# Kernel optimization log

Hardware: AMD Instinct MI355X
Metric: run time of the kernel (lower is better)

The kernel has to match this reference:

```python
import jax, jax.numpy as jnp
import numpy as np


def setup_inputs() -> dict:
    key = jax.random.key(0)
    ks = jax.random.split(key, 8)
    T, B, I, H = 512, 64, 512, 1024
    def xavier(k, shape):
        fan_in, fan_out = shape[1], shape[0]
        bound = float(np.sqrt(6.0 / (fan_in + fan_out)))
        return jax.random.uniform(k, shape, jnp.float32, -bound, bound)
    return {
        "x_seq": jax.random.normal(ks[0], (T, B, I), jnp.float32),
        "h0": jax.random.normal(ks[1], (B, H), jnp.float32),
        "U_c": xavier(ks[2], (H, I)),
        "W_c": xavier(ks[3], (H, H)),
        "b_c": jnp.zeros((H,), jnp.float32),
        "U_a": xavier(ks[4], (H, I)),
        "W_a": xavier(ks[5], (H, H)),
        "b_a": jnp.zeros((H,), jnp.float32),
        "U_h": xavier(ks[6], (H, I)),
        "b_h": jnp.zeros((H,), jnp.float32),
    }


def reference(x_seq, h0, U_c, W_c, b_c, U_a, W_a, b_a, U_h, b_h):
    # Precompute input projections for all timesteps in one big GEMM each:
    # [T, B, I] x [I, H] -> [T, B, H]
    xc = jnp.einsum('tbi,hi->tbh', x_seq, U_c) + b_c
    xa = jnp.einsum('tbi,hi->tbh', x_seq, U_a) + b_a
    xh = jnp.einsum('tbi,hi->tbh', x_seq, U_h) + b_h

    def step(h, xs):
        xc_t, xa_t, xh_t = xs
        c = jax.nn.sigmoid(xc_t + h @ W_c.T)           # [B, H]
        a = 1.0 + jnp.tanh(xa_t + h @ W_a.T)            # [B, H]
        h_new = c * h + (1.0 - c) * jnp.tanh(xh_t + a * h)
        return h_new, h_new

    h_final, y_seq = jax.lax.scan(step, h0, (xc, xa, xh))
    return y_seq, h_final
```

## Files before the change

### kernel.cpp

```cpp
#include <hip/hip_runtime.h>
#include <stdint.h>

typedef unsigned short u16;
typedef unsigned int u32;
typedef unsigned long long u64;
typedef short short8 __attribute__((ext_vector_type(8)));
typedef float f32x4 __attribute__((ext_vector_type(4)));
typedef float f32x2 __attribute__((ext_vector_type(2)));

#define T_STEPS 512
#define BATCH 64
#define IDIM 512
#define HDIM 1024
#define TBm (T_STEPS*BATCH)
#define N3 (3*HDIM)
#define NBLK 128

__device__ __forceinline__ float bf2f(u16 s) {
  union { u32 u; float f; } v; v.u = ((u32)s) << 16; return v.f;
}
__device__ __forceinline__ u16 f2b(float f) {
  union { float f; u32 u; } v; v.f = f;
  u32 u = v.u;
  u += 0x7fffu + ((u >> 16) & 1u);
  return (u16)(u >> 16);
}
__device__ __forceinline__ float ftanh(float x) {
  x = fminf(20.f, fmaxf(-20.f, x));
  float e = __expf(2.f * x);
  return (e - 1.f) / (e + 1.f);
}
__device__ __forceinline__ float fsigm(float x) {
  x = fminf(30.f, fmaxf(-30.f, x));
  return 1.f / (1.f + __expf(-x));
}

__global__ void split_f32(const float* __restrict__ src, u16* __restrict__ hi,
                          u16* __restrict__ lo, int n4) {
  int i = blockIdx.x * blockDim.x + threadIdx.x;
  if (i >= n4) return;
  float4 a = ((const float4*)src)[i];
  u16 h0 = f2b(a.x), h1 = f2b(a.y), h2 = f2b(a.z), h3 = f2b(a.w);
  u16 l0 = f2b(a.x - bf2f(h0)), l1 = f2b(a.y - bf2f(h1));
  u16 l2 = f2b(a.z - bf2f(h2)), l3 = f2b(a.w - bf2f(h3));
  uint2 hv; hv.x = (u32)h0 | ((u32)h1 << 16); hv.y = (u32)h2 | ((u32)h3 << 16);
  uint2 lv; lv.x = (u32)l0 | ((u32)l1 << 16); lv.y = (u32)l2 | ((u32)l3 << 16);
  ((uint2*)hi)[i] = hv;
  ((uint2*)lo)[i] = lv;
}

__global__ void ws_small_kernel(float* out, int n, float val) {
  int i = blockIdx.x * blockDim.x + threadIdx.x;
  for (; i < n; i += gridDim.x * blockDim.x) out[i] = val;
}

template<typename PT>
__global__ __launch_bounds__(256) void proj_gemm(const u16* __restrict__ Xh, const u16* __restrict__ Xl,
                                                 const u16* __restrict__ Uh, const u16* __restrict__ Ul,
                                                 const float* __restrict__ bias,
                                                 PT* __restrict__ Pb) {
  __shared__ u16 Ash[4096], Asl[4096], Bsh[4096], Bsl[4096];
  const int tid = threadIdx.x;
  const int bm = blockIdx.x, bn = blockIdx.y;
  const int w = tid >> 6, l = tid & 63;
  const int wm = w >> 1, wn = w & 1;
  const int lr = l & 15, kg = l >> 4;

  const int r0t = tid >> 2;
  const int kc = tid & 3;
  const size_t ga0 = (size_t)(bm * 128 + r0t) * IDIM + kc * 8;
  const size_t ga1 = ga0 + (size_t)64 * IDIM;
  const size_t gb0 = (size_t)(bn * 128 + r0t) * IDIM + kc * 8;
  const size_t gb1 = gb0 + (size_t)64 * IDIM;
  const int la0 = (kc * 128 + r0t) * 8;
  const int la1 = la0 + 64 * 8;

  uint4 rah0 = *(const uint4*)(Xh + ga0);
  uint4 rah1 = *(const uint4*)(Xh + ga1);
  uint4 ral0 = *(const uint4*)(Xl + ga0);
  uint4 ral1 = *(const uint4*)(Xl + ga1);
  uint4 rbh0 = *(const uint4*)(Uh + gb0);
  uint4 rbh1 = *(const uint4*)(Uh + gb1);
  uint4 rbl0 = *(const uint4*)(Ul + gb0);
  uint4 rbl1 = *(const uint4*)(Ul + gb1);

  const f32x4 vz = {0.f, 0.f, 0.f, 0.f};
  f32x4 acc[4][4];
#pragma unroll
  for (int i = 0; i < 4; i++)
#pragma unroll
    for (int j = 0; j < 4; j++) acc[i][j] = vz;

  for (int kt = 0; kt < 16; kt++) {
    *(uint4*)&Ash[la0] = rah0; *(uint4*)&Ash[la1] = rah1;
    *(uint4*)&Asl[la0] = ral0; *(uint4*)&Asl[la1] = ral1;
    *(uint4*)&Bsh[la0] = rbh0; *(uint4*)&Bsh[la1] = rbh1;
    *(uint4*)&Bsl[la0] = rbl0; *(uint4*)&Bsl[la1] = rbl1;
    __syncthreads();
    if (kt < 15) {
      size_t ko = (size_t)(kt + 1) * 32;
      rah0 = *(const uint4*)(Xh + ga0 + ko); rah1 = *(const uint4*)(Xh + ga1 + ko);
      ral0 = *(const uint4*)(Xl + ga0 + ko); ral1 = *(const uint4*)(Xl + ga1 + ko);
      rbh0 = *(const uint4*)(Uh + gb0 + ko); rbh1 = *(const uint4*)(Uh + gb1 + ko);
      rbl0 = *(const uint4*)(Ul + gb0 + ko); rbl1 = *(const uint4*)(Ul + gb1 + ko);
    }
    short8 afh[4], afl[4], bfh[4], bfl[4];
#pragma unroll
    for (int mt = 0; mt < 4; mt++) {
      int idx = (kg * 128 + wm * 64 + mt * 16 + lr) * 8;
      afh[mt] = *(const short8*)&Ash[idx];
      afl[mt] = *(const short8*)&Asl[idx];
    }
#pragma unroll
    for (int nt = 0; nt < 4; nt++) {
      int idx = (kg * 128 + wn * 64 + nt * 16 + lr) * 8;
      bfh[nt] = *(const short8*)&Bsh[idx];
      bfl[nt] = *(const short8*)&Bsl[idx];
    }
#pragma unroll
    for (int mt = 0; mt < 4; mt++)
#pragma unroll
      for (int nt = 0; nt < 4; nt++) {
        acc[mt][nt] = __builtin_amdgcn_mfma_f32_16x16x32_bf16(afh[mt], bfh[nt], acc[mt][nt], 0, 0, 0);
        acc[mt][nt] = __builtin_amdgcn_mfma_f32_16x16x32_bf16(afh[mt], bfl[nt], acc[mt][nt], 0, 0, 0);
        acc[mt][nt] = __builtin_amdgcn_mfma_f32_16x16x32_bf16(afl[mt], bfh[nt], acc[mt][nt], 0, 0, 0);
      }
    __syncthreads();
  }
#pragma unroll
  for (int mt = 0; mt < 4; mt++) {
#pragma unroll
    for (int nt = 0; nt < 4; nt++) {
      int col = bn * 128 + wn * 64 + nt * 16 + lr;
      float bv = bias[col];
#pragma unroll
      for (int r = 0; r < 4; r++) {
        int row = bm * 128 + wm * 64 + mt * 16 + kg * 4 + r;
        Pb[(size_t)row * N3 + col] = (PT)(acc[mt][nt][r] + bv);
      }
    }
  }
}

template<typename PT>
__global__ __launch_bounds__(512, 2) void scan_kernel(const PT* __restrict__ P,
                                                      const u16* __restrict__ Wh,
                                                      const u16* __restrict__ Wl,
                                                      const float* __restrict__ h0,
                                                      u16* __restrict__ Hh, u16* __restrict__ Hl,
                                                      u32* __restrict__ flags,
                                                      float* __restrict__ out) {
  __shared__ float ex[2][8][16][36];
  const int tid = threadIdx.x;
  const int blk = blockIdx.x;
  const int cb = blk & 31, rg = blk >> 5;
  const int c0 = cb * 32, r0 = rg * 16;
  const int w = tid >> 6, l = tid & 63;
  const int lr = l & 15, lk = l >> 4;

  short8 bwh[2][2][4], bwl[2][2][4];
#pragma unroll
  for (int m = 0; m < 2; m++)
#pragma unroll
    for (int ct = 0; ct < 2; ct++) {
      const size_t woff = ((size_t)m << 20) + (size_t)(c0 + ct * 16 + lr) * HDIM + w * 128 + lk * 8;
#pragma unroll
      for (int s = 0; s < 4; s++) {
        bwh[m][ct][s] = *(const short8*)(Wh + woff + s * 32);
        bwl[m][ct][s] = *(const short8*)(Wl + woff + s * 32);
      }
    }

  const int er = (tid & 255) >> 4;
  const int cq = tid & 15;
  const int gr = r0 + er;
  const int gc = c0 + cq * 2;
  float hs0 = 0.f, hs1 = 0.f;
  if (tid < 256) {
    hs0 = h0[(size_t)gr * HDIM + gc];
    hs1 = h0[(size_t)gr * HDIM + gc + 1];
  }

  const f32x4 vz = {0.f, 0.f, 0.f, 0.f};
  u32 budget = 1u << 20;

#pragma unroll 1
  for (int t = 0; t < T_STEPS; t++) {
    float xc0 = 0.f, xc1 = 0.f, xa0 = 0.f, xa1 = 0.f, xh0 = 0.f, xh1 = 0.f;
    if (tid < 256) {
      const PT* prow = P + (size_t)(t * BATCH + gr) * N3 + gc;
      xc0 = (float)prow[0];        xc1 = (float)prow[1];
      xa0 = (float)prow[HDIM];     xa1 = (float)prow[HDIM + 1];
      xh0 = (float)prow[2 * HDIM]; xh1 = (float)prow[2 * HDIM + 1];
    }

    if (t > 0) {
      if (tid < 64) {
        const u32* fp = flags + (size_t)t * 128 + rg * 32 + (tid & 31);
        for (;;) {
          u32 v = __hip_atomic_load(fp, __ATOMIC_RELAXED, __HIP_MEMORY_SCOPE_AGENT);
          if (__all(v != 0u) || budget == 0u) break;
          --budget;
          __builtin_amdgcn_s_sleep(1);
        }
      }
      __syncthreads();
    }

    const size_t hb = (size_t)(t & 1) * BATCH * HDIM + (size_t)(r0 + lr) * HDIM + w * 128 + lk * 8;
    short8 hH[4], hL[4];
#pragma unroll
    for (int s = 0; s < 4; s++) {
      asm volatile("global_load_dwordx4 %0, %1, off sc0 sc1"
                   : "=&v"(hH[s]) : "v"(Hh + hb + s * 32) : "memory");
      asm volatile("global_load_dwordx4 %0, %1, off sc0 sc1"
                   : "=&v"(hL[s]) : "v"(Hl + hb + s * 32) : "memory");
    }
    asm volatile("s_waitcnt vmcnt(0)" ::: "memory");
    __builtin_amdgcn_sched_barrier(0);

    f32x4 acc[2][2];
    acc[0][0] = vz; acc[0][1] = vz; acc[1][0] = vz; acc[1][1] = vz;
#pragma unroll
    for (int s = 0; s < 4; s++) {
#pragma unroll
      for (int m = 0; m < 2; m++)
#pragma unroll
        for (int ct = 0; ct < 2; ct++) {
          acc[m][ct] = __builtin_amdgcn_mfma_f32_16x16x32_bf16(hH[s], bwh[m][ct][s], acc[m][ct], 0, 0, 0);
          acc[m][ct] = __builtin_amdgcn_mfma_f32_16x16x32_bf16(hH[s], bwl[m][ct][s], acc[m][ct], 0, 0, 0);
          acc[m][ct] = __builtin_amdgcn_mfma_f32_16x16x32_bf16(hL[s], bwh[m][ct][s], acc[m][ct], 0, 0, 0);
        }
    }

#pragma unroll
    for (int m = 0; m < 2; m++)
#pragma unroll
      for (int ct = 0; ct < 2; ct++)
#pragma unroll
        for (int r = 0; r < 4; r++)
          ex[m][w][lk * 4 + r][ct * 16 + lr] = acc[m][ct][r];
    __syncthreads();

    float hn0 = 0.f, hn1 = 0.f;
    if (tid < 256) {
      const int ec = cq * 2;
      float cp0 = xc0, cp1 = xc1, ap0 = xa0, ap1 = xa1;
#pragma unroll
      for (int q = 0; q < 8; q++) {
        cp0 += ex[0][q][er][ec];     cp1 += ex[0][q][er][ec + 1];
        ap0 += ex[1][q][er][ec];     ap1 += ex[1][q][er][ec + 1];
      }
      float c0g = fsigm(cp0), c1g = fsigm(cp1);
      float aa0 = 1.f + ftanh(ap0), aa1 = 1.f + ftanh(ap1);
      float th0 = ftanh(xh0 + aa0 * hs0), th1 = ftanh(xh1 + aa1 * hs1);
      hn0 = c0g * hs0 + (1.f - c0g) * th0;
      hn1 = c1g * hs1 + (1.f - c1g) * th1;
      hs0 = hn0; hs1 = hn1;

      u16 hb_0 = f2b(hn0), hb_1 = f2b(hn1);
      u16 lb_0 = f2b(hn0 - bf2f(hb_0)), lb_1 = f2b(hn1 - bf2f(hb_1));
      size_t hidx = ((size_t)((t + 1) & 1) * BATCH * HDIM + (size_t)gr * HDIM + gc) >> 1;
      __hip_atomic_store((u32*)Hh + hidx, (u32)hb_0 | ((u32)hb_1 << 16),
                         __ATOMIC_RELAXED, __HIP_MEMORY_SCOPE_AGENT);
      __hip_atomic_store((u32*)Hl + hidx, (u32)lb_0 | ((u32)lb_1 << 16),
                         __ATOMIC_RELAXED, __HIP_MEMORY_SCOPE_AGENT);
    }

    __syncthreads();
    if (tid == 0)
      __hip_atomic_store(flags + (size_t)(t + 1) * 128 + rg * 32 + cb, 1u,
                         __ATOMIC_RELAXED, __HIP_MEMORY_SCOPE_AGENT);

    if (tid < 256) {
      float* yrow = out + (size_t)t * BATCH * HDIM + (size_t)gr * HDIM + gc;
      f32x2 y = {hn0, hn1};
      __builtin_nontemporal_store(y, (f32x2*)yrow);
      if (t == T_STEPS - 1) {
        float* frow = out + (size_t)T_STEPS * BATCH * HDIM + (size_t)gr * HDIM + gc;
        __builtin_nontemporal_store(y, (f32x2*)frow);
      }
    }
  }
}

static const size_t SZ_X1 = (size_t)TBm * IDIM * 2;
static const size_t SZ_U1 = (size_t)N3 * IDIM * 2;
static const size_t SZ_W1 = (size_t)2 * HDIM * HDIM * 2;
static const size_t SZ_B  = (size_t)N3 * 4;
static const size_t SZ_H1 = (size_t)2 * BATCH * HDIM * 2;
static const size_t SZ_C  = (size_t)(T_STEPS + 1) * 128 * 4;
static const size_t SZ_TAIL = 2*SZ_X1 + 2*SZ_U1 + 2*SZ_W1 + SZ_B + 2*SZ_H1 + SZ_C;

template<typename PT>
static void launch_path(void* const* d_in, float* out, char* ws, hipStream_t stream) {
  const float* x_seq = (const float*)d_in[0];
  const float* h0   = (const float*)d_in[1];
  const float* U_c  = (const float*)d_in[2];
  const float* W_c  = (const float*)d_in[3];
  const float* b_c  = (const float*)d_in[4];
  const float* U_a  = (const float*)d_in[5];
  const float* W_a  = (const float*)d_in[6];
  const float* b_a  = (const float*)d_in[7];
  const float* U_h  = (const float*)d_in[8];
  const float* b_h  = (const float*)d_in[9];

  const size_t szP = (size_t)TBm * N3 * sizeof(PT);
  PT*  Pb  = (PT*)(ws);
  u16* Xh  = (u16*)(ws + szP);
  u16* Xl  = (u16*)(ws + szP + SZ_X1);
  u16* Uh  = (u16*)(ws + szP + 2*SZ_X1);
  u16* Ul  = (u16*)(ws + szP + 2*SZ_X1 + SZ_U1);
  u16* Wh  = (u16*)(ws + szP + 2*SZ_X1 + 2*SZ_U1);
  u16* Wl  = (u16*)(ws + szP + 2*SZ_X1 + 2*SZ_U1 + SZ_W1);
  float* bias = (float*)(ws + szP + 2*SZ_X1 + 2*SZ_U1 + 2*SZ_W1);
  u16* Hh  = (u16*)((char*)bias + SZ_B);
  u16* Hl  = (u16*)((char*)bias + SZ_B + SZ_H1);
  u32* Fl  = (u32*)((char*)bias + SZ_B + 2*SZ_H1);

  (void)hipMemsetAsync(Fl, 0, SZ_C, stream);
  (void)hipMemcpyAsync(bias + 0 * HDIM, b_c, HDIM * sizeof(float), hipMemcpyDeviceToDevice, stream);
  (void)hipMemcpyAsync(bias + 1 * HDIM, b_a, HDIM * sizeof(float), hipMemcpyDeviceToDevice, stream);
  (void)hipMemcpyAsync(bias + 2 * HDIM, b_h, HDIM * sizeof(float), hipMemcpyDeviceToDevice, stream);

  int n4;
  n4 = TBm * IDIM / 4;
  split_f32<<<(n4 + 255) / 256, 256, 0, stream>>>(x_seq, Xh, Xl, n4);
  n4 = HDIM * IDIM / 4;
  split_f32<<<(n4 + 255) / 256, 256, 0, stream>>>(U_c, Uh + 0 * (size_t)HDIM * IDIM, Ul + 0 * (size_t)HDIM * IDIM, n4);
  split_f32<<<(n4 + 255) / 256, 256, 0, stream>>>(U_a, Uh + 1 * (size_t)HDIM * IDIM, Ul + 1 * (size_t)HDIM * IDIM, n4);
  split_f32<<<(n4 + 255) / 256, 256, 0, stream>>>(U_h, Uh + 2 * (size_t)HDIM * IDIM, Ul + 2 * (size_t)HDIM * IDIM, n4);
  n4 = HDIM * HDIM / 4;
  split_f32<<<(n4 + 255) / 256, 256, 0, stream>>>(W_c, Wh, Wl, n4);
  split_f32<<<(n4 + 255) / 256, 256, 0, stream>>>(W_a, Wh + (size_t)HDIM * HDIM, Wl + (size_t)HDIM * HDIM, n4);
  n4 = BATCH * HDIM / 4;
  split_f32<<<(n4 + 255) / 256, 256, 0, stream>>>(h0, Hh, Hl, n4);

  proj_gemm<PT><<<dim3(TBm / 128, N3 / 128), 256, 0, stream>>>(Xh, Xl, Uh, Ul, bias, Pb);
  scan_kernel<PT><<<NBLK, 512, 0, stream>>>(Pb, Wh, Wl, h0, Hh, Hl, Fl, out);
}

extern "C" void kernel_launch(void* const* d_in, const int* in_sizes, int n_in,
                              void* d_out, int out_size, void* d_ws, size_t ws_size,
                              hipStream_t stream) {
  const size_t need_f32 = (size_t)TBm * N3 * 4 + SZ_TAIL;
  const size_t need_f16 = (size_t)TBm * N3 * 2 + SZ_TAIL;

  if (ws_size >= need_f32) {
    launch_path<float>(d_in, (float*)d_out, (char*)d_ws, stream);
  } else if (ws_size >= need_f16) {
    launch_path<_Float16>(d_in, (float*)d_out, (char*)d_ws, stream);
  } else {
    float v = 1.0e6f + (float)(ws_size >> 20);
    ws_small_kernel<<<2048, 256, 0, stream>>>((float*)d_out, out_size, v);
  }
}
```

Before: 2.473 ms.

## Replace flag-based step sync with tagged hidden-state words polled directly

The hidden state is now packed into one 32-bit word per element: the bf16 hi part, a truncated lo part, and a 3-bit step tag in the low bits. Consumers spin on the hidden-state loads themselves until every tag matches the current step. This removes the separate flag array, the flag store with its extra barrier, and the dependent flag-poll-then-load round trip on each of the 512 sequential steps. In exchange the lo part loses 3 mantissa bits, each poll reloads the whole h tile, and launch bounds are relaxed to one block per CU.

```diff
diff --git a/kernel.cpp b/kernel.cpp
--- a/kernel.cpp
+++ b/kernel.cpp
@@ -5,6 +5,7 @@
 typedef unsigned int u32;
 typedef unsigned long long u64;
 typedef short short8 __attribute__((ext_vector_type(8)));
+typedef unsigned int u32x4 __attribute__((ext_vector_type(4)));
 typedef float f32x4 __attribute__((ext_vector_type(4)));
 typedef float f32x2 __attribute__((ext_vector_type(2)));
 
@@ -49,6 +50,14 @@
   ((uint2*)lo)[i] = lv;
 }
 
+__global__ void init_h(const float* __restrict__ h0, u32* __restrict__ Hs) {
+  int i = blockIdx.x * blockDim.x + threadIdx.x;
+  float v = h0[i];
+  u16 hb = f2b(v);
+  u16 lb = f2b(v - bf2f(hb));
+  Hs[i] = ((u32)hb << 16) | (u32)(lb & 0xFFF8u);
+}
+
 __global__ void ws_small_kernel(float* out, int n, float val) {
   int i = blockIdx.x * blockDim.x + threadIdx.x;
   for (; i < n; i += gridDim.x * blockDim.x) out[i] = val;
@@ -143,12 +152,11 @@
 }
 
 template<typename PT>
-__global__ __launch_bounds__(512, 2) void scan_kernel(const PT* __restrict__ P,
+__global__ __launch_bounds__(512, 1) void scan_kernel(const PT* __restrict__ P,
                                                       const u16* __restrict__ Wh,
                                                       const u16* __restrict__ Wl,
                                                       const float* __restrict__ h0,
-                                                      u16* __restrict__ Hh, u16* __restrict__ Hl,
-                                                      u32* __restrict__ flags,
+                                                      u32* __restrict__ Hs,
                                                       float* __restrict__ out) {
   __shared__ float ex[2][8][16][36];
   const int tid = threadIdx.x;
@@ -182,7 +190,7 @@
   }
 
   const f32x4 vz = {0.f, 0.f, 0.f, 0.f};
-  u32 budget = 1u << 20;
+  u32 budget = 1u << 18;
 
 #pragma unroll 1
   for (int t = 0; t < T_STEPS; t++) {
@@ -194,30 +202,44 @@
       xh0 = (float)prow[2 * HDIM]; xh1 = (float)prow[2 * HDIM + 1];
     }
 
-    if (t > 0) {
-      if (tid < 64) {
-        const u32* fp = flags + (size_t)t * 128 + rg * 32 + (tid & 31);
-        for (;;) {
-          u32 v = __hip_atomic_load(fp, __ATOMIC_RELAXED, __HIP_MEMORY_SCOPE_AGENT);
-          if (__all(v != 0u) || budget == 0u) break;
-          --budget;
-          __builtin_amdgcn_s_sleep(1);
-        }
-      }
-      __syncthreads();
-    }
-
-    const size_t hb = (size_t)(t & 1) * BATCH * HDIM + (size_t)(r0 + lr) * HDIM + w * 128 + lk * 8;
+    const u32* hp = Hs + ((size_t)(t & 1) << 16) + (size_t)(r0 + lr) * HDIM + w * 128 + lk * 8;
+    u32x4 pw[8];
+    const u32 want = (u32)(t & 7);
+    for (;;) {
+#pragma unroll
+      for (int s = 0; s < 4; s++) {
+        asm volatile("global_load_dwordx4 %0, %1, off sc0 sc1"
+                     : "=&v"(pw[2 * s]) : "v"(hp + s * 32) : "memory");
+        asm volatile("global_load_dwordx4 %0, %1, off sc0 sc1"
+                     : "=&v"(pw[2 * s + 1]) : "v"(hp + s * 32 + 4) : "memory");
+      }
+      asm volatile("s_waitcnt vmcnt(0)" ::: "memory");
+      bool ok = true;
+#pragma unroll
+      for (int i = 0; i < 8; i++)
+#pragma unroll
+        for (int j = 0; j < 4; j++) ok &= ((pw[i][j] & 7u) == want);
+      if (__all(ok) || --budget == 0u) break;
+      __builtin_amdgcn_s_sleep(1);
+    }
+    __builtin_amdgcn_sched_barrier(0);
+
     short8 hH[4], hL[4];
 #pragma unroll
     for (int s = 0; s < 4; s++) {
-      asm volatile("global_load_dwordx4 %0, %1, off sc0 sc1"
-                   : "=&v"(hH[s]) : "v"(Hh + hb + s * 32) : "memory");
-      asm volatile("global_load_dwordx4 %0, %1, off sc0 sc1"
-                   : "=&v"(hL[s]) : "v"(Hl + hb + s * 32) : "memory");
-    }
-    asm volatile("s_waitcnt vmcnt(0)" ::: "memory");
-    __builtin_amdgcn_sched_barrier(0);
+      u32x4 a = pw[2 * s], b = pw[2 * s + 1];
+      union { u32x4 u; short8 v; } uh, ul;
+      uh.u[0] = (a[0] >> 16) | (a[1] & 0xFFFF0000u);
+      uh.u[1] = (a[2] >> 16) | (a[3] & 0xFFFF0000u);
+      uh.u[2] = (b[0] >> 16) | (b[1] & 0xFFFF0000u);
+      uh.u[3] = (b[2] >> 16) | (b[3] & 0xFFFF0000u);
+      ul.u[0] = (a[0] & 0xFFF8u) | ((a[1] & 0xFFF8u) << 16);
+      ul.u[1] = (a[2] & 0xFFF8u) | ((a[3] & 0xFFF8u) << 16);
+      ul.u[2] = (b[0] & 0xFFF8u) | ((b[1] & 0xFFF8u) << 16);
+      ul.u[3] = (b[2] & 0xFFF8u) | ((b[3] & 0xFFF8u) << 16);
+      hH[s] = uh.v;
+      hL[s] = ul.v;
+    }
 
     f32x4 acc[2][2];
     acc[0][0] = vz; acc[0][1] = vz; acc[1][0] = vz; acc[1][1] = vz;
@@ -233,6 +255,8 @@
         }
     }
 
+    __syncthreads();
+
 #pragma unroll
     for (int m = 0; m < 2; m++)
 #pragma unroll
@@ -242,7 +266,6 @@
           ex[m][w][lk * 4 + r][ct * 16 + lr] = acc[m][ct][r];
     __syncthreads();
 
-    float hn0 = 0.f, hn1 = 0.f;
     if (tid < 256) {
       const int ec = cq * 2;
       float cp0 = xc0, cp1 = xc1, ap0 = xa0, ap1 = xa1;
@@ -254,25 +277,19 @@
       float c0g = fsigm(cp0), c1g = fsigm(cp1);
       float aa0 = 1.f + ftanh(ap0), aa1 = 1.f + ftanh(ap1);
       float th0 = ftanh(xh0 + aa0 * hs0), th1 = ftanh(xh1 + aa1 * hs1);
-      hn0 = c0g * hs0 + (1.f - c0g) * th0;
-      hn1 = c1g * hs1 + (1.f - c1g) * th1;
+      float hn0 = c0g * hs0 + (1.f - c0g) * th0;
+      float hn1 = c1g * hs1 + (1.f - c1g) * th1;
       hs0 = hn0; hs1 = hn1;
 
+      const u32 tagn = (u32)((t + 1) & 7);
       u16 hb_0 = f2b(hn0), hb_1 = f2b(hn1);
       u16 lb_0 = f2b(hn0 - bf2f(hb_0)), lb_1 = f2b(hn1 - bf2f(hb_1));
-      size_t hidx = ((size_t)((t + 1) & 1) * BATCH * HDIM + (size_t)gr * HDIM + gc) >> 1;
-      __hip_atomic_store((u32*)Hh + hidx, (u32)hb_0 | ((u32)hb_1 << 16),
-                         __ATOMIC_RELAXED, __HIP_MEMORY_SCOPE_AGENT);
-      __hip_atomic_store((u32*)Hl + hidx, (u32)lb_0 | ((u32)lb_1 << 16),
-                         __ATOMIC_RELAXED, __HIP_MEMORY_SCOPE_AGENT);
-    }
-
-    __syncthreads();
-    if (tid == 0)
-      __hip_atomic_store(flags + (size_t)(t + 1) * 128 + rg * 32 + cb, 1u,
-                         __ATOMIC_RELAXED, __HIP_MEMORY_SCOPE_AGENT);
-
-    if (tid < 256) {
+      u32 w0 = ((u32)hb_0 << 16) | (u32)(lb_0 & 0xFFF8u) | tagn;
+      u32 w1 = ((u32)hb_1 << 16) | (u32)(lb_1 & 0xFFF8u) | tagn;
+      u64 wq = (u64)w0 | ((u64)w1 << 32);
+      u64* hdst = (u64*)(Hs + ((size_t)((t + 1) & 1) << 16) + (size_t)gr * HDIM + gc);
+      __hip_atomic_store(hdst, wq, __ATOMIC_RELAXED, __HIP_MEMORY_SCOPE_AGENT);
+
       float* yrow = out + (size_t)t * BATCH * HDIM + (size_t)gr * HDIM + gc;
       f32x2 y = {hn0, hn1};
       __builtin_nontemporal_store(y, (f32x2*)yrow);
@@ -288,9 +305,8 @@
 static const size_t SZ_U1 = (size_t)N3 * IDIM * 2;
 static const size_t SZ_W1 = (size_t)2 * HDIM * HDIM * 2;
 static const size_t SZ_B  = (size_t)N3 * 4;
-static const size_t SZ_H1 = (size_t)2 * BATCH * HDIM * 2;
-static const size_t SZ_C  = (size_t)(T_STEPS + 1) * 128 * 4;
-static const size_t SZ_TAIL = 2*SZ_X1 + 2*SZ_U1 + 2*SZ_W1 + SZ_B + 2*SZ_H1 + SZ_C;
+static const size_t SZ_HS = (size_t)2 * BATCH * HDIM * 4;
+static const size_t SZ_TAIL = 2*SZ_X1 + 2*SZ_U1 + 2*SZ_W1 + SZ_B + SZ_HS;
 
 template<typename PT>
 static void launch_path(void* const* d_in, float* out, char* ws, hipStream_t stream) {
@@ -314,11 +330,8 @@
   u16* Wh  = (u16*)(ws + szP + 2*SZ_X1 + 2*SZ_U1);
   u16* Wl  = (u16*)(ws + szP + 2*SZ_X1 + 2*SZ_U1 + SZ_W1);
   float* bias = (float*)(ws + szP + 2*SZ_X1 + 2*SZ_U1 + 2*SZ_W1);
-  u16* Hh  = (u16*)((char*)bias + SZ_B);
-  u16* Hl  = (u16*)((char*)bias + SZ_B + SZ_H1);
-  u32* Fl  = (u32*)((char*)bias + SZ_B + 2*SZ_H1);
-
-  (void)hipMemsetAsync(Fl, 0, SZ_C, stream);
+  u32* Hs  = (u32*)((char*)bias + SZ_B);
+
   (void)hipMemcpyAsync(bias + 0 * HDIM, b_c, HDIM * sizeof(float), hipMemcpyDeviceToDevice, stream);
   (void)hipMemcpyAsync(bias + 1 * HDIM, b_a, HDIM * sizeof(float), hipMemcpyDeviceToDevice, stream);
   (void)hipMemcpyAsync(bias + 2 * HDIM, b_h, HDIM * sizeof(float), hipMemcpyDeviceToDevice, stream);
@@ -333,11 +346,11 @@
   n4 = HDIM * HDIM / 4;
   split_f32<<<(n4 + 255) / 256, 256, 0, stream>>>(W_c, Wh, Wl, n4);
   split_f32<<<(n4 + 255) / 256, 256, 0, stream>>>(W_a, Wh + (size_t)HDIM * HDIM, Wl + (size_t)HDIM * HDIM, n4);
-  n4 = BATCH * HDIM / 4;
-  split_f32<<<(n4 + 255) / 256, 256, 0, stream>>>(h0, Hh, Hl, n4);
+
+  init_h<<<(BATCH * HDIM) / 256, 256, 0, stream>>>(h0, Hs);
 
   proj_gemm<PT><<<dim3(TBm / 128, N3 / 128), 256, 0, stream>>>(Xh, Xl, Uh, Ul, bias, Pb);
-  scan_kernel<PT><<<NBLK, 512, 0, stream>>>(Pb, Wh, Wl, h0, Hh, Hl, Fl, out);
+  scan_kernel<PT><<<NBLK, 512, 0, stream>>>(Pb, Wh, Wl, h0, Hs, out);
 }
 
 extern "C" void kernel_launch(void* const* d_in, const int* in_sizes, int n_in,
```

Result: slower. 3.860 ms (+56.1%).

## Fuse projection GEMM into scan kernel with per-row-tile readiness counters

Applied to the files above, without the earlier changes.

Merges the input-projection GEMM and the recurrent scan into one launch. The first 128 blocks run the scan and the remaining blocks compute projection tiles, each of which bumps a per-row-tile counter when done. Scan blocks then spin on both the step flags and the projection counter for the current timestep, so the serial scan can start while later projections are still being computed. The projection tile work is reshaped to 512 threads with 4x2 warps, stores and loads use cache-bypassing sc0 sc1, and the f16 fallback path is dropped. The risks are that 1-block-per-CU occupancy (96KB of LDS) slows the GEMM, and that scan blocks could wait on projection blocks that are never scheduled.

```diff
diff --git a/kernel.cpp b/kernel.cpp
--- a/kernel.cpp
+++ b/kernel.cpp
@@ -15,6 +15,7 @@
 #define TBm (T_STEPS*BATCH)
 #define N3 (3*HDIM)
 #define NBLK 128
+#define PROJ_BLKS (256*24)
 
 __device__ __forceinline__ float bf2f(u16 s) {
   union { u32 u; float f; } v; v.u = ((u32)s) << 16; return v.f;
@@ -54,109 +55,104 @@
   for (; i < n; i += gridDim.x * blockDim.x) out[i] = val;
 }
 
-template<typename PT>
-__global__ __launch_bounds__(256) void proj_gemm(const u16* __restrict__ Xh, const u16* __restrict__ Xl,
-                                                 const u16* __restrict__ Uh, const u16* __restrict__ Ul,
-                                                 const float* __restrict__ bias,
-                                                 PT* __restrict__ Pb) {
-  __shared__ u16 Ash[4096], Asl[4096], Bsh[4096], Bsl[4096];
+__global__ __launch_bounds__(512, 1) void fused_kernel(
+    const u16* __restrict__ Xh, const u16* __restrict__ Xl,
+    const u16* __restrict__ Uh, const u16* __restrict__ Ul,
+    const u16* __restrict__ Wh, const u16* __restrict__ Wl,
+    const float* __restrict__ bias, const float* __restrict__ h0,
+    float* __restrict__ Pb, u16* __restrict__ Hh, u16* __restrict__ Hl,
+    u32* __restrict__ flags, u32* __restrict__ pcnt, float* __restrict__ out) {
+  __shared__ __align__(16) char smem[98304];
   const int tid = threadIdx.x;
-  const int bm = blockIdx.x, bn = blockIdx.y;
   const int w = tid >> 6, l = tid & 63;
-  const int wm = w >> 1, wn = w & 1;
-  const int lr = l & 15, kg = l >> 4;
-
-  const int r0t = tid >> 2;
-  const int kc = tid & 3;
-  const size_t ga0 = (size_t)(bm * 128 + r0t) * IDIM + kc * 8;
-  const size_t ga1 = ga0 + (size_t)64 * IDIM;
-  const size_t gb0 = (size_t)(bn * 128 + r0t) * IDIM + kc * 8;
-  const size_t gb1 = gb0 + (size_t)64 * IDIM;
-  const int la0 = (kc * 128 + r0t) * 8;
-  const int la1 = la0 + 64 * 8;
-
-  uint4 rah0 = *(const uint4*)(Xh + ga0);
-  uint4 rah1 = *(const uint4*)(Xh + ga1);
-  uint4 ral0 = *(const uint4*)(Xl + ga0);
-  uint4 ral1 = *(const uint4*)(Xl + ga1);
-  uint4 rbh0 = *(const uint4*)(Uh + gb0);
-  uint4 rbh1 = *(const uint4*)(Uh + gb1);
-  uint4 rbl0 = *(const uint4*)(Ul + gb0);
-  uint4 rbl1 = *(const uint4*)(Ul + gb1);
-
+  const int lr = l & 15, lk = l >> 4;
   const f32x4 vz = {0.f, 0.f, 0.f, 0.f};
-  f32x4 acc[4][4];
-#pragma unroll
-  for (int i = 0; i < 4; i++)
-#pragma unroll
-    for (int j = 0; j < 4; j++) acc[i][j] = vz;
-
-  for (int kt = 0; kt < 16; kt++) {
-    *(uint4*)&Ash[la0] = rah0; *(uint4*)&Ash[la1] = rah1;
-    *(uint4*)&Asl[la0] = ral0; *(uint4*)&Asl[la1] = ral1;
-    *(uint4*)&Bsh[la0] = rbh0; *(uint4*)&Bsh[la1] = rbh1;
-    *(uint4*)&Bsl[la0] = rbl0; *(uint4*)&Bsl[la1] = rbl1;
+
+  if (blockIdx.x >= NBLK) {
+    const int pid = blockIdx.x - NBLK;
+    const int bm = pid / 24, bn = pid % 24;
+    u16* Ash = (u16*)smem;
+    u16* Asl = Ash + 4096;
+    u16* Bsh = Asl + 4096;
+    u16* Bsl = Bsh + 4096;
+    const int wm = w >> 2, wn = w & 3;
+    const int r0t = tid >> 2, kc = tid & 3;
+
+    const size_t ga = (size_t)(bm * 128 + r0t) * IDIM + kc * 8;
+    const size_t gb = (size_t)(bn * 128 + r0t) * IDIM + kc * 8;
+    const int la = (kc * 128 + r0t) * 8;
+
+    uint4 rah = *(const uint4*)(Xh + ga);
+    uint4 ral = *(const uint4*)(Xl + ga);
+    uint4 rbh = *(const uint4*)(Uh + gb);
+    uint4 rbl = *(const uint4*)(Ul + gb);
+
+    f32x4 acc[4][2];
+#pragma unroll
+    for (int i = 0; i < 4; i++) { acc[i][0] = vz; acc[i][1] = vz; }
+
+    for (int kt = 0; kt < 16; kt++) {
+      *(uint4*)&Ash[la] = rah;
+      *(uint4*)&Asl[la] = ral;
+      *(uint4*)&Bsh[la] = rbh;
+      *(uint4*)&Bsl[la] = rbl;
+      __syncthreads();
+      if (kt < 15) {
+        size_t ko = (size_t)(kt + 1) * 32;
+        rah = *(const uint4*)(Xh + ga + ko);
+        ral = *(const uint4*)(Xl + ga + ko);
+        rbh = *(const uint4*)(Uh + gb + ko);
+        rbl = *(const uint4*)(Ul + gb + ko);
+      }
+      short8 afh[4], afl[4], bfh[2], bfl[2];
+#pragma unroll
+      for (int mt = 0; mt < 4; mt++) {
+        int idx = (lk * 128 + wm * 64 + mt * 16 + lr) * 8;
+        afh[mt] = *(const short8*)&Ash[idx];
+        afl[mt] = *(const short8*)&Asl[idx];
+      }
+#pragma unroll
+      for (int nt = 0; nt < 2; nt++) {
+        int idx = (lk * 128 + wn * 32 + nt * 16 + lr) * 8;
+        bfh[nt] = *(const short8*)&Bsh[idx];
+        bfl[nt] = *(const short8*)&Bsl[idx];
+      }
+#pragma unroll
+      for (int mt = 0; mt < 4; mt++)
+#pragma unroll
+        for (int nt = 0; nt < 2; nt++) {
+          acc[mt][nt] = __builtin_amdgcn_mfma_f32_16x16x32_bf16(afh[mt], bfh[nt], acc[mt][nt], 0, 0, 0);
+          acc[mt][nt] = __builtin_amdgcn_mfma_f32_16x16x32_bf16(afh[mt], bfl[nt], acc[mt][nt], 0, 0, 0);
+          acc[mt][nt] = __builtin_amdgcn_mfma_f32_16x16x32_bf16(afl[mt], bfh[nt], acc[mt][nt], 0, 0, 0);
+        }
+      __syncthreads();
+    }
+#pragma unroll
+    for (int mt = 0; mt < 4; mt++)
+#pragma unroll
+      for (int nt = 0; nt < 2; nt++) {
+        int col = bn * 128 + wn * 32 + nt * 16 + lr;
+        float bv = bias[col];
+#pragma unroll
+        for (int r = 0; r < 4; r++) {
+          int row = bm * 128 + wm * 64 + mt * 16 + lk * 4 + r;
+          float val = acc[mt][nt][r] + bv;
+          asm volatile("global_store_dword %0, %1, off sc0 sc1"
+                       :: "v"(Pb + (size_t)row * N3 + col), "v"(val) : "memory");
+        }
+      }
+    asm volatile("s_waitcnt vmcnt(0)" ::: "memory");
     __syncthreads();
-    if (kt < 15) {
-      size_t ko = (size_t)(kt + 1) * 32;
-      rah0 = *(const uint4*)(Xh + ga0 + ko); rah1 = *(const uint4*)(Xh + ga1 + ko);
-      ral0 = *(const uint4*)(Xl + ga0 + ko); ral1 = *(const uint4*)(Xl + ga1 + ko);
-      rbh0 = *(const uint4*)(Uh + gb0 + ko); rbh1 = *(const uint4*)(Uh + gb1 + ko);
-      rbl0 = *(const uint4*)(Ul + gb0 + ko); rbl1 = *(const uint4*)(Ul + gb1 + ko);
-    }
-    short8 afh[4], afl[4], bfh[4], bfl[4];
-#pragma unroll
-    for (int mt = 0; mt < 4; mt++) {
-      int idx = (kg * 128 + wm * 64 + mt * 16 + lr) * 8;
-      afh[mt] = *(const short8*)&Ash[idx];
-      afl[mt] = *(const short8*)&Asl[idx];
-    }
-#pragma unroll
-    for (int nt = 0; nt < 4; nt++) {
-      int idx = (kg * 128 + wn * 64 + nt * 16 + lr) * 8;
-      bfh[nt] = *(const short8*)&Bsh[idx];
-      bfl[nt] = *(const short8*)&Bsl[idx];
-    }
-#pragma unroll
-    for (int mt = 0; mt < 4; mt++)
-#pragma unroll
-      for (int nt = 0; nt < 4; nt++) {
-        acc[mt][nt] = __builtin_amdgcn_mfma_f32_16x16x32_bf16(afh[mt], bfh[nt], acc[mt][nt], 0, 0, 0);
-        acc[mt][nt] = __builtin_amdgcn_mfma_f32_16x16x32_bf16(afh[mt], bfl[nt], acc[mt][nt], 0, 0, 0);
-        acc[mt][nt] = __builtin_amdgcn_mfma_f32_16x16x32_bf16(afl[mt], bfh[nt], acc[mt][nt], 0, 0, 0);
-      }
-    __syncthreads();
+    if (tid == 0)
+      (void)__hip_atomic_fetch_add(pcnt + (size_t)bm * 32, 1u,
+                                   __ATOMIC_RELAXED, __HIP_MEMORY_SCOPE_AGENT);
+    return;
   }
-#pragma unroll
-  for (int mt = 0; mt < 4; mt++) {
-#pragma unroll
-    for (int nt = 0; nt < 4; nt++) {
-      int col = bn * 128 + wn * 64 + nt * 16 + lr;
-      float bv = bias[col];
-#pragma unroll
-      for (int r = 0; r < 4; r++) {
-        int row = bm * 128 + wm * 64 + mt * 16 + kg * 4 + r;
-        Pb[(size_t)row * N3 + col] = (PT)(acc[mt][nt][r] + bv);
-      }
-    }
-  }
-}
-
-template<typename PT>
-__global__ __launch_bounds__(512, 2) void scan_kernel(const PT* __restrict__ P,
-                                                      const u16* __restrict__ Wh,
-                                                      const u16* __restrict__ Wl,
-                                                      const float* __restrict__ h0,
-                                                      u16* __restrict__ Hh, u16* __restrict__ Hl,
-                                                      u32* __restrict__ flags,
-                                                      float* __restrict__ out) {
-  __shared__ float ex[2][8][16][36];
-  const int tid = threadIdx.x;
+
+  auto ex = (float (*)[8][16][36])smem;
   const int blk = blockIdx.x;
   const int cb = blk & 31, rg = blk >> 5;
   const int c0 = cb * 32, r0 = rg * 16;
-  const int w = tid >> 6, l = tid & 63;
-  const int lr = l & 15, lk = l >> 4;
 
   short8 bwh[2][2][4], bwl[2][2][4];
 #pragma unroll
@@ -181,30 +177,32 @@
     hs1 = h0[(size_t)gr * HDIM + gc + 1];
   }
 
-  const f32x4 vz = {0.f, 0.f, 0.f, 0.f};
   u32 budget = 1u << 20;
 
 #pragma unroll 1
   for (int t = 0; t < T_STEPS; t++) {
-    float xc0 = 0.f, xc1 = 0.f, xa0 = 0.f, xa1 = 0.f, xh0 = 0.f, xh1 = 0.f;
+    if (tid < 64) {
+      const u32* fp = flags + (size_t)t * 128 + rg * 32 + (l & 31);
+      const u32* pc = pcnt + (size_t)(t >> 1) * 32;
+      for (;;) {
+        u32 v;
+        if (l < 32)
+          v = (t == 0) ? 1u : __hip_atomic_load(fp, __ATOMIC_RELAXED, __HIP_MEMORY_SCOPE_AGENT);
+        else
+          v = (__hip_atomic_load(pc, __ATOMIC_RELAXED, __HIP_MEMORY_SCOPE_AGENT) == 24u) ? 1u : 0u;
+        if (__all(v != 0u) || budget == 0u) break;
+        --budget;
+        __builtin_amdgcn_s_sleep(1);
+      }
+    }
+    __syncthreads();
+
+    f32x2 pc2, pa2, ph2;
+    const float* prow = Pb + (size_t)(t * BATCH + gr) * N3 + gc;
     if (tid < 256) {
-      const PT* prow = P + (size_t)(t * BATCH + gr) * N3 + gc;
-      xc0 = (float)prow[0];        xc1 = (float)prow[1];
-      xa0 = (float)prow[HDIM];     xa1 = (float)prow[HDIM + 1];
-      xh0 = (float)prow[2 * HDIM]; xh1 = (float)prow[2 * HDIM + 1];
-    }
-
-    if (t > 0) {
-      if (tid < 64) {
-        const u32* fp = flags + (size_t)t * 128 + rg * 32 + (tid & 31);
-        for (;;) {
-          u32 v = __hip_atomic_load(fp, __ATOMIC_RELAXED, __HIP_MEMORY_SCOPE_AGENT);
-          if (__all(v != 0u) || budget == 0u) break;
-          --budget;
-          __builtin_amdgcn_s_sleep(1);
-        }
-      }
-      __syncthreads();
+      asm volatile("global_load_dwordx2 %0, %1, off sc0 sc1" : "=&v"(pc2) : "v"(prow) : "memory");
+      asm volatile("global_load_dwordx2 %0, %1, off sc0 sc1" : "=&v"(pa2) : "v"(prow + HDIM) : "memory");
+      asm volatile("global_load_dwordx2 %0, %1, off sc0 sc1" : "=&v"(ph2) : "v"(prow + 2 * HDIM) : "memory");
     }
 
     const size_t hb = (size_t)(t & 1) * BATCH * HDIM + (size_t)(r0 + lr) * HDIM + w * 128 + lk * 8;
@@ -245,7 +243,7 @@
     float hn0 = 0.f, hn1 = 0.f;
     if (tid < 256) {
       const int ec = cq * 2;
-      float cp0 = xc0, cp1 = xc1, ap0 = xa0, ap1 = xa1;
+      float cp0 = pc2[0], cp1 = pc2[1], ap0 = pa2[0], ap1 = pa2[1];
 #pragma unroll
       for (int q = 0; q < 8; q++) {
         cp0 += ex[0][q][er][ec];     cp1 += ex[0][q][er][ec + 1];
@@ -253,7 +251,7 @@
       }
       float c0g = fsigm(cp0), c1g = fsigm(cp1);
       float aa0 = 1.f + ftanh(ap0), aa1 = 1.f + ftanh(ap1);
-      float th0 = ftanh(xh0 + aa0 * hs0), th1 = ftanh(xh1 + aa1 * hs1);
+      float th0 = ftanh(ph2[0] + aa0 * hs0), th1 = ftanh(ph2[1] + aa1 * hs1);
       hn0 = c0g * hs0 + (1.f - c0g) * th0;
       hn1 = c1g * hs1 + (1.f - c1g) * th1;
       hs0 = hn0; hs1 = hn1;
@@ -284,16 +282,19 @@
   }
 }
 
+static const size_t SZ_P  = (size_t)TBm * N3 * 4;
 static const size_t SZ_X1 = (size_t)TBm * IDIM * 2;
 static const size_t SZ_U1 = (size_t)N3 * IDIM * 2;
 static const size_t SZ_W1 = (size_t)2 * HDIM * HDIM * 2;
 static const size_t SZ_B  = (size_t)N3 * 4;
 static const size_t SZ_H1 = (size_t)2 * BATCH * HDIM * 2;
-static const size_t SZ_C  = (size_t)(T_STEPS + 1) * 128 * 4;
-static const size_t SZ_TAIL = 2*SZ_X1 + 2*SZ_U1 + 2*SZ_W1 + SZ_B + 2*SZ_H1 + SZ_C;
-
-template<typename PT>
-static void launch_path(void* const* d_in, float* out, char* ws, hipStream_t stream) {
+static const size_t SZ_F  = (size_t)(T_STEPS + 1) * 128 * 4;
+static const size_t SZ_PC = (size_t)256 * 32 * 4;
+static const size_t WS_NEED = SZ_P + 2*SZ_X1 + 2*SZ_U1 + 2*SZ_W1 + SZ_B + 2*SZ_H1 + SZ_F + SZ_PC;
+
+extern "C" void kernel_launch(void* const* d_in, const int* in_sizes, int n_in,
+                              void* d_out, int out_size, void* d_ws, size_t ws_size,
+                              hipStream_t stream) {
   const float* x_seq = (const float*)d_in[0];
   const float* h0   = (const float*)d_in[1];
   const float* U_c  = (const float*)d_in[2];
@@ -305,20 +306,27 @@
   const float* U_h  = (const float*)d_in[8];
   const float* b_h  = (const float*)d_in[9];
 
-  const size_t szP = (size_t)TBm * N3 * sizeof(PT);
-  PT*  Pb  = (PT*)(ws);
-  u16* Xh  = (u16*)(ws + szP);
-  u16* Xl  = (u16*)(ws + szP + SZ_X1);
-  u16* Uh  = (u16*)(ws + szP + 2*SZ_X1);
-  u16* Ul  = (u16*)(ws + szP + 2*SZ_X1 + SZ_U1);
-  u16* Wh  = (u16*)(ws + szP + 2*SZ_X1 + 2*SZ_U1);
-  u16* Wl  = (u16*)(ws + szP + 2*SZ_X1 + 2*SZ_U1 + SZ_W1);
-  float* bias = (float*)(ws + szP + 2*SZ_X1 + 2*SZ_U1 + 2*SZ_W1);
+  if (ws_size < WS_NEED) {
+    float v = 1.0e6f + (float)(ws_size >> 20);
+    ws_small_kernel<<<2048, 256, 0, stream>>>((float*)d_out, out_size, v);
+    return;
+  }
+
+  char* ws = (char*)d_ws;
+  float* Pb = (float*)(ws);
+  u16* Xh  = (u16*)(ws + SZ_P);
+  u16* Xl  = (u16*)(ws + SZ_P + SZ_X1);
+  u16* Uh  = (u16*)(ws + SZ_P + 2*SZ_X1);
+  u16* Ul  = (u16*)(ws + SZ_P + 2*SZ_X1 + SZ_U1);
+  u16* Wh  = (u16*)(ws + SZ_P + 2*SZ_X1 + 2*SZ_U1);
+  u16* Wl  = (u16*)(ws + SZ_P + 2*SZ_X1 + 2*SZ_U1 + SZ_W1);
+  float* bias = (float*)(ws + SZ_P + 2*SZ_X1 + 2*SZ_U1 + 2*SZ_W1);
   u16* Hh  = (u16*)((char*)bias + SZ_B);
   u16* Hl  = (u16*)((char*)bias + SZ_B + SZ_H1);
   u32* Fl  = (u32*)((char*)bias + SZ_B + 2*SZ_H1);
-
-  (void)hipMemsetAsync(Fl, 0, SZ_C, stream);
+  u32* Pc  = (u32*)((char*)bias + SZ_B + 2*SZ_H1 + SZ_F);
+
+  (void)hipMemsetAsync(Fl, 0, SZ_F + SZ_PC, stream);
   (void)hipMemcpyAsync(bias + 0 * HDIM, b_c, HDIM * sizeof(float), hipMemcpyDeviceToDevice, stream);
   (void)hipMemcpyAsync(bias + 1 * HDIM, b_a, HDIM * sizeof(float), hipMemcpyDeviceToDevice, stream);
   (void)hipMemcpyAsync(bias + 2 * HDIM, b_h, HDIM * sizeof(float), hipMemcpyDeviceToDevice, stream);
@@ -336,22 +344,6 @@
   n4 = BATCH * HDIM / 4;
   split_f32<<<(n4 + 255) / 256, 256, 0, stream>>>(h0, Hh, Hl, n4);
 
-  proj_gemm<PT><<<dim3(TBm / 128, N3 / 128), 256, 0, stream>>>(Xh, Xl, Uh, Ul, bias, Pb);
-  scan_kernel<PT><<<NBLK, 512, 0, stream>>>(Pb, Wh, Wl, h0, Hh, Hl, Fl, out);
-}
-
-extern "C" void kernel_launch(void* const* d_in, const int* in_sizes, int n_in,
-                              void* d_out, int out_size, void* d_ws, size_t ws_size,
-                              hipStream_t stream) {
-  const size_t need_f32 = (size_t)TBm * N3 * 4 + SZ_TAIL;
-  const size_t need_f16 = (size_t)TBm * N3 * 2 + SZ_TAIL;
-
-  if (ws_size >= need_f32) {
-    launch_path<float>(d_in, (float*)d_out, (char*)d_ws, stream);
-  } else if (ws_size >= need_f16) {
-    launch_path<_Float16>(d_in, (float*)d_out, (char*)d_ws, stream);
-  } else {
-    float v = 1.0e6f + (float)(ws_size >> 20);
-    ws_small_kernel<<<2048, 256, 0, stream>>>((float*)d_out, out_size, v);
-  }
-}
+  fused_kernel<<<NBLK + PROJ_BLKS, 512, 0, stream>>>(Xh, Xl, Uh, Ul, Wh, Wl, bias, h0,
+                                                     Pb, Hh, Hl, Fl, Pc, (float*)d_out);
+}
```

Result: faster. 2.246 ms (-9.2%).
